# Optimization experiments

Hardware: AMD Instinct MI355X
Metric: run time of the kernel (lower is better)

The kernel has to match this reference:

```python
import jax, jax.numpy as jnp
import numpy as np

TOP_K = 2  # num_experts_per_token


def setup_inputs() -> dict:
    key = jax.random.key(0)
    k1, k2, k3, k4 = jax.random.split(key, 4)
    B, S, D, F, E = 2, 2048, 1024, 4096, 8
    hidden_states = jax.random.normal(k1, (B, S, D), dtype=jnp.float32)
    # router: nn.Linear(D, E, bias=False) -> weight [E, D]
    Wr = jax.random.normal(k2, (E, D), dtype=jnp.float32) * (1.0 / np.sqrt(D))
    # expert FFNs: W1 [E, D, F] (first Linear, transposed), W2 [E, F, D]
    W1 = jax.random.normal(k3, (E, D, F), dtype=jnp.float32) * (1.0 / np.sqrt(D))
    W2 = jax.random.normal(k4, (E, F, D), dtype=jnp.float32) * (1.0 / np.sqrt(F))
    return {"hidden_states": hidden_states, "Wr": Wr, "W1": W1, "W2": W2}


def reference(hidden_states, Wr, W1, W2):
    B, S, D = hidden_states.shape
    E = Wr.shape[0]
    x = hidden_states.reshape(-1, D)                      # [T, D]
    T = x.shape[0]

    router_logits = x @ Wr.T                              # [T, E]
    routing_weights = jax.nn.softmax(router_logits, axis=-1)
    top_w, top_idx = jax.lax.top_k(routing_weights, TOP_K)  # [T, K]
    top_w = top_w / jnp.sum(top_w, axis=-1, keepdims=True)

    # combine weights scattered into dense [T, E] (zero for unselected experts)
    comb = jnp.zeros((T, E), dtype=x.dtype).at[
        jnp.arange(T)[:, None], top_idx
    ].add(top_w)

    # per-expert FFN: SiLU(x @ W1) @ W2, computed densely then masked-combined
    h = jax.nn.silu(jnp.einsum('td,edf->tef', x, W1))     # [T, E, F]
    y = jnp.einsum('tef,efd->ted', h, W2)                 # [T, E, D]
    out = jnp.einsum('te,ted->td', comb, y)               # [T, D]
    return out.reshape(B, S, D)
```

## Files before the change

kernel.cpp:

```cpp
#include <hip/hip_runtime.h>
#include <hip/hip_bf16.h>

#define T_TOK 4096
#define DDIM  1024
#define FDIM  4096
#define NEXP  8
#define TLMAX 136

typedef __attribute__((ext_vector_type(8))) short bf16x8;
typedef __attribute__((ext_vector_type(4))) float f32x4;

__device__ __forceinline__ void gl2lds16(const void* g, void* l) {
  __builtin_amdgcn_global_load_lds((const __attribute__((address_space(1))) void*)g,
                                   (__attribute__((address_space(3))) void*)l,
                                   16, 0, 0);
}

__device__ __forceinline__ unsigned short f2bf(float f) {
  unsigned u = __float_as_uint(f);
  unsigned r = (u + 0x7fffu + ((u >> 16) & 1u)) >> 16;
  return (unsigned short)r;
}
__device__ __forceinline__ float bf2f(unsigned short u) {
  return __uint_as_float((unsigned)u << 16);
}

__global__ __launch_bounds__(256) void moe_router(
    const float* __restrict__ x, const float* __restrict__ Wr,
    unsigned short* __restrict__ xb, int* __restrict__ te, float* __restrict__ tw) {
  __shared__ float wr[NEXP * DDIM];
  const int tid = threadIdx.x;
#pragma unroll
  for (int i = 0; i < NEXP * DDIM / 256; ++i) wr[i * 256 + tid] = Wr[i * 256 + tid];
  __syncthreads();

  const int wave = tid >> 6, lane = tid & 63;
  const int t = blockIdx.x * 4 + wave;
  const float* xr = x + (size_t)t * DDIM;
  const int d0 = lane * 16;

  float4 xv[4];
#pragma unroll
  for (int j = 0; j < 4; ++j) xv[j] = *(const float4*)(xr + d0 + j * 4);

  float lg[NEXP];
#pragma unroll
  for (int e = 0; e < NEXP; ++e) {
    float s = 0.f;
#pragma unroll
    for (int j = 0; j < 4; ++j) {
      float4 wv = *(const float4*)(&wr[e * DDIM + d0 + j * 4]);
      s += xv[j].x * wv.x + xv[j].y * wv.y + xv[j].z * wv.z + xv[j].w * wv.w;
    }
    lg[e] = s;
  }
#pragma unroll
  for (int e = 0; e < NEXP; ++e) {
#pragma unroll
    for (int off = 32; off > 0; off >>= 1) lg[e] += __shfl_xor(lg[e], off);
  }

#pragma unroll
  for (int j = 0; j < 4; ++j) {
    ushort4 o;
    o.x = f2bf(xv[j].x); o.y = f2bf(xv[j].y); o.z = f2bf(xv[j].z); o.w = f2bf(xv[j].w);
    *(ushort4*)(xb + (size_t)t * DDIM + d0 + j * 4) = o;
  }

  if (lane == 0) {
    int i0 = 0;
#pragma unroll
    for (int e = 1; e < NEXP; ++e) if (lg[e] > lg[i0]) i0 = e;
    int i1 = (i0 == 0) ? 1 : 0;
#pragma unroll
    for (int e = 0; e < NEXP; ++e) if (e != i0 && lg[e] > lg[i1]) i1 = e;
    float w0 = 1.f / (1.f + __expf(lg[i1] - lg[i0]));
    te[t * 2 + 0] = i0; te[t * 2 + 1] = i1;
    tw[t * 2 + 0] = w0; tw[t * 2 + 1] = 1.f - w0;
  }
}

__global__ __launch_bounds__(256) void moe_count(const int* __restrict__ te,
                                                 int* __restrict__ counts) {
  __shared__ int lh[NEXP];
  const int tid = threadIdx.x;
  if (tid < NEXP) lh[tid] = 0;
  __syncthreads();
  const int t = blockIdx.x * 256 + tid;
  atomicAdd(&lh[te[t * 2 + 0]], 1);
  atomicAdd(&lh[te[t * 2 + 1]], 1);
  __syncthreads();
  if (tid < NEXP) atomicAdd(&counts[tid], lh[tid]);
}

__global__ void moe_prefix(const int* __restrict__ counts, int* __restrict__ offs,
                           int* __restrict__ fill, int* __restrict__ tcnt,
                           int* __restrict__ tlist) {
  if (threadIdx.x == 0) {
    int s = 0, tt = 0;
    for (int e = 0; e < NEXP; ++e) {
      offs[e] = s;
      int c = counts[e];
      s += c;
      fill[e] = 0;
      for (int mt = 0; mt * 64 < c; ++mt) tlist[tt++] = (e << 8) | mt;
    }
    offs[NEXP] = s;
    tcnt[0] = tt;
  }
}

__global__ __launch_bounds__(256) void moe_scatter(
    const int* __restrict__ te, const int* __restrict__ offs, int* __restrict__ fill,
    int* __restrict__ rows, int* __restrict__ slot) {
  __shared__ int lcnt[NEXP], lbase[NEXP];
  const int tid = threadIdx.x;
  if (tid < NEXP) lcnt[tid] = 0;
  __syncthreads();
  const int t = blockIdx.x * 256 + tid;
  const int e0 = te[t * 2 + 0], e1 = te[t * 2 + 1];
  const int r0 = atomicAdd(&lcnt[e0], 1);
  const int r1 = atomicAdd(&lcnt[e1], 1);
  __syncthreads();
  if (tid < NEXP) lbase[tid] = atomicAdd(&fill[tid], lcnt[tid]);
  __syncthreads();
  int p0 = offs[e0] + lbase[e0] + r0;
  int p1 = offs[e1] + lbase[e1] + r1;
  rows[p0] = t; rows[p1] = t;
  slot[t * 2 + 0] = p0; slot[t * 2 + 1] = p1;
}

__global__ __launch_bounds__(256) void wconv_t(const float* __restrict__ W,
                                               unsigned short* __restrict__ Wt,
                                               int K, int N) {
  __shared__ unsigned short t[64][65];
  const int e = blockIdx.z;
  const float* src = W + (size_t)e * K * N + (size_t)(blockIdx.y * 64) * N + blockIdx.x * 64;
  unsigned short* dst = Wt + (size_t)e * N * K + (size_t)(blockIdx.x * 64) * K + blockIdx.y * 64;
  const int tid = threadIdx.x;
  const int rr = tid >> 4;
  const int cc4 = (tid & 15) * 4;
#pragma unroll
  for (int i = 0; i < 4; ++i) {
    int r = i * 16 + rr;
    float4 v = *(const float4*)(src + (size_t)r * N + cc4);
    t[cc4 + 0][r] = f2bf(v.x);
    t[cc4 + 1][r] = f2bf(v.y);
    t[cc4 + 2][r] = f2bf(v.z);
    t[cc4 + 3][r] = f2bf(v.w);
  }
  __syncthreads();
  const int k8 = (tid & 7) * 8;
#pragma unroll
  for (int i = 0; i < 2; ++i) {
    int c = i * 32 + (tid >> 3);
    uint4 pk;
    pk.x = (unsigned)t[c][k8 + 0] | ((unsigned)t[c][k8 + 1] << 16);
    pk.y = (unsigned)t[c][k8 + 2] | ((unsigned)t[c][k8 + 3] << 16);
    pk.z = (unsigned)t[c][k8 + 4] | ((unsigned)t[c][k8 + 5] << 16);
    pk.w = (unsigned)t[c][k8 + 6] | ((unsigned)t[c][k8 + 7] << 16);
    *(uint4*)(dst + (size_t)c * K + k8) = pk;
  }
}

template <int KD, int KSLICE, int ND, bool GATHER, bool DOSILU>
__global__ __launch_bounds__(512, 4) void moe_gemm(
    const unsigned short* __restrict__ Asrc, const unsigned short* __restrict__ Wt,
    const int* __restrict__ rows, const int* __restrict__ offs,
    const int* __restrict__ tcnt, const int* __restrict__ tlist,
    unsigned short* __restrict__ Out) {
  constexpr int BM = 64, BN = 256;
  constexpr int S = KD / KSLICE;
  constexpr int NTN = ND / BN;
  constexpr int NPAN = NTN * S;
  constexpr int NB = TLMAX * NPAN;
  constexpr int CB = BN / 64;
  constexpr int MF = BM / 32, NF = 4;

  __shared__ alignas(16) unsigned short Alds[2][BM * 64];
  __shared__ alignas(16) unsigned short Blds[2][BN * 64];

  const int bid = blockIdx.x;
  const int orig = (bid & 7) * (NB >> 3) + (bid >> 3);
  const int TT = tcnt[0];
  if (orig >= TT * NPAN) return;
  const int tt = orig % TT;
  const int panel = orig / TT;
  const int nt = panel % NTN;
  const int ksl = panel / NTN;
  const int pk = tlist[tt];
  const int e = pk >> 8, mt = pk & 255;

  const int base = offs[e];
  const int cnt = offs[e + 1] - base;
  const int m0 = mt * BM;
  const int valid = min(BM, cnt - m0);
  const size_t koff = (size_t)ksl * KSLICE;

  const int tid = threadIdx.x;
  const int w = tid >> 6, lane = tid & 63;
  const int wm = w >> 2, wn = w & 3;

  const int n0 = nt * BN;
  const unsigned short* Wb = Wt + (size_t)e * ND * KD + (size_t)n0 * KD + koff;

  const int cc8 = ((lane & 7) ^ (lane >> 3)) * 8;
  const int ar = w * 8 + (lane >> 3);
  const int aslot = base + m0 + min(ar, valid - 1);
  const size_t aoff = (size_t)(GATHER ? rows[aslot] : aslot) * KD + koff + cc8;
  size_t boff[CB];
#pragma unroll
  for (int s = 0; s < CB; ++s) {
    int r = s * 64 + w * 8 + (lane >> 3);
    boff[s] = (size_t)r * KD + cc8;
  }

  f32x4 acc[MF][NF] = {};

#define STAGE(b, k0)                                                         \
  {                                                                          \
    gl2lds16(Asrc + aoff + (k0), &Alds[b][w * 512]);                         \
    _Pragma("unroll") for (int s = 0; s < CB; ++s)                           \
        gl2lds16(Wb + boff[s] + (k0), &Blds[b][(s * 512 + w * 64) * 8]);     \
  }

#define COMPUTE(b)                                                           \
  {                                                                          \
    _Pragma("unroll") for (int ks = 0; ks < 2; ++ks) {                       \
      bf16x8 af[MF], bfr[NF];                                                \
      _Pragma("unroll") for (int mf = 0; mf < MF; ++mf) {                    \
        int row = wm * 32 + mf * 16 + (lane & 15);                           \
        int cc = ks * 4 + (lane >> 4);                                       \
        af[mf] = *(const bf16x8*)((const char*)&Alds[b][0] + row * 128 +     \
                                  ((cc ^ (row & 7)) * 16));                  \
      }                                                                      \
      _Pragma("unroll") for (int nf = 0; nf < NF; ++nf) {                    \
        int col = wn * 64 + nf * 16 + (lane & 15);                           \
        int cc = ks * 4 + (lane >> 4);                                       \
        bfr[nf] = *(const bf16x8*)((const char*)&Blds[b][0] + col * 128 +    \
                                   ((cc ^ (col & 7)) * 16));                 \
      }                                                                      \
      _Pragma("unroll") for (int mf = 0; mf < MF; ++mf)                      \
          _Pragma("unroll") for (int nf = 0; nf < NF; ++nf)                  \
              acc[mf][nf] = __builtin_amdgcn_mfma_f32_16x16x32_bf16(         \
                  af[mf], bfr[nf], acc[mf][nf], 0, 0, 0);                    \
    }                                                                        \
  }

  constexpr int NK = KSLICE / 64;
  STAGE(0, 0);
  for (int t = 0; t < NK; t += 2) {
    STAGE(1, (t + 1) * 64);
    asm volatile("s_waitcnt vmcnt(5)" ::: "memory");
    __builtin_amdgcn_s_barrier();
    COMPUTE(0);
    __builtin_amdgcn_s_barrier();
    if (t + 2 < NK) {
      STAGE(0, (t + 2) * 64);
      asm volatile("s_waitcnt vmcnt(5)" ::: "memory");
    } else {
      asm volatile("s_waitcnt vmcnt(0)" ::: "memory");
    }
    __builtin_amdgcn_s_barrier();
    COMPUTE(1);
    __builtin_amdgcn_s_barrier();
  }
#undef STAGE
#undef COMPUTE

  unsigned short* Op = Out + (size_t)ksl * 8192 * ND;
  const int q = lane >> 4, c16 = lane & 15;
#pragma unroll
  for (int mf = 0; mf < MF; ++mf) {
#pragma unroll
    for (int r = 0; r < 4; ++r) {
      int lrow = wm * 32 + mf * 16 + q * 4 + r;
      if (lrow < valid) {
#pragma unroll
        for (int nf = 0; nf < NF; ++nf) {
          int gcol = n0 + wn * 64 + nf * 16 + c16;
          float v = acc[mf][nf][r];
          if (DOSILU) v = v / (1.f + __expf(-v));
          Op[(size_t)(base + m0 + lrow) * ND + gcol] = f2bf(v);
        }
      }
    }
  }
}

__global__ __launch_bounds__(256) void moe_combine(
    const unsigned short* __restrict__ y, const int* __restrict__ slot,
    const float* __restrict__ tw, float* __restrict__ out) {
  const int t = blockIdx.x;
  const int s0 = slot[t * 2], s1 = slot[t * 2 + 1];
  const float w0 = tw[t * 2], w1 = tw[t * 2 + 1];
  const int i = threadIdx.x * 4;
  ushort4 a = *(const ushort4*)(y + (size_t)s0 * DDIM + i);
  ushort4 b = *(const ushort4*)(y + (size_t)(8192 + s0) * DDIM + i);
  ushort4 c = *(const ushort4*)(y + (size_t)s1 * DDIM + i);
  ushort4 d = *(const ushort4*)(y + (size_t)(8192 + s1) * DDIM + i);
  float4 r;
  r.x = w0 * (bf2f(a.x) + bf2f(b.x)) + w1 * (bf2f(c.x) + bf2f(d.x));
  r.y = w0 * (bf2f(a.y) + bf2f(b.y)) + w1 * (bf2f(c.y) + bf2f(d.y));
  r.z = w0 * (bf2f(a.z) + bf2f(b.z)) + w1 * (bf2f(c.z) + bf2f(d.z));
  r.w = w0 * (bf2f(a.w) + bf2f(b.w)) + w1 * (bf2f(c.w) + bf2f(d.w));
  *(float4*)(out + (size_t)t * DDIM + i) = r;
}

extern "C" void kernel_launch(void* const* d_in, const int* in_sizes, int n_in,
                              void* d_out, int out_size, void* d_ws, size_t ws_size,
                              hipStream_t stream) {
  const float* x  = (const float*)d_in[0];
  const float* Wr = (const float*)d_in[1];
  const float* W1 = (const float*)d_in[2];
  const float* W2 = (const float*)d_in[3];
  float* out = (float*)d_out;

  char* ws = (char*)d_ws;
  unsigned short* xb = (unsigned short*)ws;
  unsigned short* H  = (unsigned short*)(ws + (size_t)(8 << 20));
  unsigned short* WT = (unsigned short*)(ws + (size_t)(72 << 20));
  unsigned short* y  = (unsigned short*)(ws + (size_t)(136 << 20));
  char* meta = ws + (size_t)(168 << 20);
  int* rows   = (int*)meta;
  int* te     = (int*)(meta + (32 << 10));
  float* tw   = (float*)(meta + (64 << 10));
  int* slot   = (int*)(meta + (96 << 10));
  int* counts = (int*)(meta + (128 << 10));
  int* offs   = counts + 16;
  int* fill   = counts + 32;
  int* tcnt   = counts + 48;
  int* tlist  = counts + 64;

  hipMemsetAsync(counts, 0, 256, stream);

  moe_router<<<T_TOK / 4, 256, 0, stream>>>(x, Wr, xb, te, tw);
  moe_count<<<T_TOK / 256, 256, 0, stream>>>(te, counts);
  moe_prefix<<<1, 64, 0, stream>>>(counts, offs, fill, tcnt, tlist);
  moe_scatter<<<T_TOK / 256, 256, 0, stream>>>(te, offs, fill, rows, slot);

  wconv_t<<<dim3(FDIM / 64, DDIM / 64, NEXP), 256, 0, stream>>>(W1, WT, DDIM, FDIM);
  moe_gemm<DDIM, DDIM, FDIM, true, true>
      <<<TLMAX * (FDIM / 256), 512, 0, stream>>>(xb, WT, rows, offs, tcnt, tlist, H);

  wconv_t<<<dim3(DDIM / 64, FDIM / 64, NEXP), 256, 0, stream>>>(W2, WT, FDIM, DDIM);
  moe_gemm<FDIM, FDIM / 2, DDIM, false, false>
      <<<TLMAX * (DDIM / 256) * 2, 512, 0, stream>>>(H, WT, nullptr, offs, tcnt, tlist, y);

  moe_combine<<<T_TOK, 256, 0, stream>>>(y, slot, tw, out);
}
```

Measured before the change: 310.8 us.

## Fuse routing count/prefix/scatter into one block and split GEMM compute phases with setprio

Measured after the change: 326.1 us. 1.05x slower.

```diff
diff --git a/kernel.cpp b/kernel.cpp
--- a/kernel.cpp
+++ b/kernel.cpp
@@ -80,54 +80,55 @@
   }
 }
 
-__global__ __launch_bounds__(256) void moe_count(const int* __restrict__ te,
-                                                 int* __restrict__ counts) {
-  __shared__ int lh[NEXP];
+__global__ __launch_bounds__(1024) void moe_route_fused(
+    const int* __restrict__ te, int* __restrict__ offs_g,
+    int* __restrict__ tcnt, int* __restrict__ tlist,
+    int* __restrict__ rows, int* __restrict__ slot) {
+  __shared__ int cnt[NEXP], ofl[NEXP], fil[NEXP];
   const int tid = threadIdx.x;
-  if (tid < NEXP) lh[tid] = 0;
-  __syncthreads();
-  const int t = blockIdx.x * 256 + tid;
-  atomicAdd(&lh[te[t * 2 + 0]], 1);
-  atomicAdd(&lh[te[t * 2 + 1]], 1);
-  __syncthreads();
-  if (tid < NEXP) atomicAdd(&counts[tid], lh[tid]);
-}
-
-__global__ void moe_prefix(const int* __restrict__ counts, int* __restrict__ offs,
-                           int* __restrict__ fill, int* __restrict__ tcnt,
-                           int* __restrict__ tlist) {
-  if (threadIdx.x == 0) {
+  const int lane = tid & 63;
+  if (tid < NEXP) { cnt[tid] = 0; fil[tid] = 0; }
+  __syncthreads();
+  int el[8];
+#pragma unroll
+  for (int r = 0; r < 8; ++r) el[r] = te[r * 1024 + tid];
+#pragma unroll
+  for (int r = 0; r < 8; ++r) {
+#pragma unroll
+    for (int ex = 0; ex < NEXP; ++ex) {
+      unsigned long long m = __ballot(el[r] == ex);
+      if (lane == ex) { int c = __popcll(m); if (c) atomicAdd(&cnt[ex], c); }
+    }
+  }
+  __syncthreads();
+  if (tid == 0) {
     int s = 0, tt = 0;
     for (int e = 0; e < NEXP; ++e) {
-      offs[e] = s;
-      int c = counts[e];
-      s += c;
-      fill[e] = 0;
+      ofl[e] = s; offs_g[e] = s;
+      int c = cnt[e]; s += c;
       for (int mt = 0; mt * 64 < c; ++mt) tlist[tt++] = (e << 8) | mt;
     }
-    offs[NEXP] = s;
+    offs_g[NEXP] = s;
     tcnt[0] = tt;
   }
-}
-
-__global__ __launch_bounds__(256) void moe_scatter(
-    const int* __restrict__ te, const int* __restrict__ offs, int* __restrict__ fill,
-    int* __restrict__ rows, int* __restrict__ slot) {
-  __shared__ int lcnt[NEXP], lbase[NEXP];
-  const int tid = threadIdx.x;
-  if (tid < NEXP) lcnt[tid] = 0;
-  __syncthreads();
-  const int t = blockIdx.x * 256 + tid;
-  const int e0 = te[t * 2 + 0], e1 = te[t * 2 + 1];
-  const int r0 = atomicAdd(&lcnt[e0], 1);
-  const int r1 = atomicAdd(&lcnt[e1], 1);
-  __syncthreads();
-  if (tid < NEXP) lbase[tid] = atomicAdd(&fill[tid], lcnt[tid]);
-  __syncthreads();
-  int p0 = offs[e0] + lbase[e0] + r0;
-  int p1 = offs[e1] + lbase[e1] + r1;
-  rows[p0] = t; rows[p1] = t;
-  slot[t * 2 + 0] = p0; slot[t * 2 + 1] = p1;
+  __syncthreads();
+#pragma unroll
+  for (int r = 0; r < 8; ++r) {
+    int e = el[r];
+    int rank = 0, wbase = 0;
+#pragma unroll
+    for (int ex = 0; ex < NEXP; ++ex) {
+      unsigned long long m = __ballot(e == ex);
+      int b = 0;
+      if (lane == ex) { int c = __popcll(m); if (c) b = atomicAdd(&fil[ex], c); }
+      b = __shfl(b, ex);
+      if (e == ex) { rank = __popcll(m & ((1ull << lane) - 1)); wbase = b; }
+    }
+    int idx = r * 1024 + tid;
+    int pos = ofl[e] + wbase + rank;
+    rows[pos] = idx >> 1;
+    slot[idx] = pos;
+  }
 }
 
 __global__ __launch_bounds__(256) void wconv_t(const float* __restrict__ W,
@@ -224,27 +225,27 @@
         gl2lds16(Wb + boff[s] + (k0), &Blds[b][(s * 512 + w * 64) * 8]);     \
   }
 
-#define COMPUTE(b)                                                           \
+#define PHASE(b, ksv)                                                        \
   {                                                                          \
-    _Pragma("unroll") for (int ks = 0; ks < 2; ++ks) {                       \
-      bf16x8 af[MF], bfr[NF];                                                \
-      _Pragma("unroll") for (int mf = 0; mf < MF; ++mf) {                    \
-        int row = wm * 32 + mf * 16 + (lane & 15);                           \
-        int cc = ks * 4 + (lane >> 4);                                       \
-        af[mf] = *(const bf16x8*)((const char*)&Alds[b][0] + row * 128 +     \
-                                  ((cc ^ (row & 7)) * 16));                  \
-      }                                                                      \
-      _Pragma("unroll") for (int nf = 0; nf < NF; ++nf) {                    \
-        int col = wn * 64 + nf * 16 + (lane & 15);                           \
-        int cc = ks * 4 + (lane >> 4);                                       \
-        bfr[nf] = *(const bf16x8*)((const char*)&Blds[b][0] + col * 128 +    \
-                                   ((cc ^ (col & 7)) * 16));                 \
-      }                                                                      \
-      _Pragma("unroll") for (int mf = 0; mf < MF; ++mf)                      \
-          _Pragma("unroll") for (int nf = 0; nf < NF; ++nf)                  \
-              acc[mf][nf] = __builtin_amdgcn_mfma_f32_16x16x32_bf16(         \
-                  af[mf], bfr[nf], acc[mf][nf], 0, 0, 0);                    \
+    bf16x8 af[MF], bfr[NF];                                                  \
+    _Pragma("unroll") for (int mf = 0; mf < MF; ++mf) {                      \
+      int row = wm * 32 + mf * 16 + (lane & 15);                             \
+      int cc = (ksv) * 4 + (lane >> 4);                                      \
+      af[mf] = *(const bf16x8*)((const char*)&Alds[b][0] + row * 128 +       \
+                                ((cc ^ (row & 7)) * 16));                    \
     }                                                                        \
+    _Pragma("unroll") for (int nf = 0; nf < NF; ++nf) {                      \
+      int col = wn * 64 + nf * 16 + (lane & 15);                             \
+      int cc = (ksv) * 4 + (lane >> 4);                                      \
+      bfr[nf] = *(const bf16x8*)((const char*)&Blds[b][0] + col * 128 +      \
+                                 ((cc ^ (col & 7)) * 16));                   \
+    }                                                                        \
+    __builtin_amdgcn_s_setprio(1);                                           \
+    _Pragma("unroll") for (int mf = 0; mf < MF; ++mf)                        \
+        _Pragma("unroll") for (int nf = 0; nf < NF; ++nf)                    \
+            acc[mf][nf] = __builtin_amdgcn_mfma_f32_16x16x32_bf16(           \
+                af[mf], bfr[nf], acc[mf][nf], 0, 0, 0);                      \
+    __builtin_amdgcn_s_setprio(0);                                           \
   }
 
   constexpr int NK = KSLICE / 64;
@@ -253,7 +254,9 @@
     STAGE(1, (t + 1) * 64);
     asm volatile("s_waitcnt vmcnt(5)" ::: "memory");
     __builtin_amdgcn_s_barrier();
-    COMPUTE(0);
+    PHASE(0, 0);
+    __builtin_amdgcn_s_barrier();
+    PHASE(0, 1);
     __builtin_amdgcn_s_barrier();
     if (t + 2 < NK) {
       STAGE(0, (t + 2) * 64);
@@ -262,11 +265,13 @@
       asm volatile("s_waitcnt vmcnt(0)" ::: "memory");
     }
     __builtin_amdgcn_s_barrier();
-    COMPUTE(1);
+    PHASE(1, 0);
+    __builtin_amdgcn_s_barrier();
+    PHASE(1, 1);
     __builtin_amdgcn_s_barrier();
   }
 #undef STAGE
-#undef COMPUTE
+#undef PHASE
 
   unsigned short* Op = Out + (size_t)ksl * 8192 * ND;
   const int q = lane >> 4, c16 = lane & 15;
@@ -326,18 +331,12 @@
   int* te     = (int*)(meta + (32 << 10));
   float* tw   = (float*)(meta + (64 << 10));
   int* slot   = (int*)(meta + (96 << 10));
-  int* counts = (int*)(meta + (128 << 10));
-  int* offs   = counts + 16;
-  int* fill   = counts + 32;
-  int* tcnt   = counts + 48;
-  int* tlist  = counts + 64;
-
-  hipMemsetAsync(counts, 0, 256, stream);
+  int* offs   = (int*)(meta + (128 << 10));
+  int* tcnt   = offs + 16;
+  int* tlist  = offs + 32;
 
   moe_router<<<T_TOK / 4, 256, 0, stream>>>(x, Wr, xb, te, tw);
-  moe_count<<<T_TOK / 256, 256, 0, stream>>>(te, counts);
-  moe_prefix<<<1, 64, 0, stream>>>(counts, offs, fill, tcnt, tlist);
-  moe_scatter<<<T_TOK / 256, 256, 0, stream>>>(te, offs, fill, rows, slot);
+  moe_route_fused<<<1, 1024, 0, stream>>>(te, offs, tcnt, tlist, rows, slot);
 
   wconv_t<<<dim3(FDIM / 64, DDIM / 64, NEXP), 256, 0, stream>>>(W1, WT, DDIM, FDIM);
   moe_gemm<DDIM, DDIM, FDIM, true, true>
```
